# Kernel optimization log

Hardware: AMD Instinct MI355X
Metric: run time of the kernel (lower is better)

The kernel has to match this reference:

```python
import jax, jax.numpy as jnp
import numpy as np

EPS = 1e-5

def setup_inputs() -> dict:
    key = jax.random.key(0)
    ks = jax.random.split(key, 8)
    B, T, D, S = 8, 4096, 1024, 64
    return {
        "x": jax.random.normal(ks[0], (B, T, D), dtype=jnp.float32),
        "time_decay": jax.random.normal(ks[1], (S,), dtype=jnp.float32) * 0.1 - 0.5,
        "time_first": jax.random.normal(ks[2], (S,), dtype=jnp.float32) * 0.1,
        "W_key": jax.random.normal(ks[3], (S, D), dtype=jnp.float32) * 0.02,
        "W_value": jax.random.normal(ks[4], (S, D), dtype=jnp.float32) * 0.02,
        "W_output": jax.random.normal(ks[5], (D, S), dtype=jnp.float32) * 0.02,
        "W_shift": jax.random.normal(ks[6], (D, D), dtype=jnp.float32) * 0.02,
        "shift_gate": jnp.ones((D,), dtype=jnp.float32),
        "ln_w": jnp.ones((D,), dtype=jnp.float32),
        "ln_b": jnp.zeros((D,), dtype=jnp.float32),
    }


def _forward(x, time_decay, time_first, W_key, W_value, W_output, W_shift, shift_gate, ln_w, ln_b):
    B, T, D = x.shape
    S = time_decay.shape[0]
    # --- token shift: rotate sequence by shift_len, project, gated blend ---
    shift_len = max(1, int(T * 0.5))
    x_cat = jnp.concatenate([x[:, shift_len:], x[:, :-shift_len]], axis=1)  # (B,T,D)
    gate = jax.nn.sigmoid(shift_gate)
    x_shift = jnp.einsum('btd,ed->bte', x_cat, W_shift) * gate + x * (1.0 - gate)
    # --- layernorm (torch: biased variance, eps=1e-5) ---
    mu = jnp.mean(x_shift, axis=-1, keepdims=True)
    var = jnp.mean(jnp.square(x_shift - mu), axis=-1, keepdims=True)
    xn = (x_shift - mu) * jax.lax.rsqrt(var + EPS) * ln_w + ln_b
    # --- key/value projections and per-step wkv (fully vectorized) ---
    k = jnp.einsum('btd,sd->bts', xn, W_key)    # (B,T,S)
    v = jnp.einsum('btd,sd->bts', xn, W_value)  # (B,T,S)
    wkv = jnp.exp(-jnp.exp(time_first) * jax.nn.sigmoid(k)) * v  # (B,T,S)
    # --- linear recurrence: state = state*w + wkv_t, scanned over T ---
    w = jnp.exp(time_decay)  # (S,)
    def step(state, wkv_t):
        state = state * w + wkv_t
        return state, state
    init = jnp.zeros((B, S), dtype=x.dtype)
    last_state, states = jax.lax.scan(step, init, jnp.swapaxes(wkv, 0, 1))  # states: (T,B,S)
    states = jnp.swapaxes(states, 0, 1)  # (B,T,S)
    # --- batched output projection (applied per-step in torch; same math) ---
    output = jnp.einsum('bts,ds->btd', states, W_output)  # (B,T,D)
    return output, last_state


def reference(x, time_decay, time_first, W_key, W_value, W_output, W_shift, shift_gate, ln_w, ln_b):
    out, last_state = _forward(x, time_decay, time_first, W_key, W_value, W_output, W_shift, shift_gate, ln_w, ln_b)
    return out, jax.lax.stop_gradient(last_state)
```

## Files before the change

kernel.cpp:

```cpp
#include <hip/hip_runtime.h>
#include <stdint.h>

#define B_ 8
#define T_ 4096
#define D_ 1024
#define S_ 64
#define N_ 32768
#define OUT_ELEMS 33554432
#define NCHK 128
#define CHKL 32

typedef __attribute__((ext_vector_type(8))) short bf16x8;
typedef __attribute__((ext_vector_type(8))) unsigned short u16x8;
typedef __attribute__((ext_vector_type(4))) float f32x4;

__device__ __forceinline__ uint16_t f2bf(float f) {
    union { float f; uint32_t u; } v; v.f = f;
    uint32_t r = v.u + 0x7FFFu + ((v.u >> 16) & 1u);
    return (uint16_t)(r >> 16);
}
__device__ __forceinline__ float bf2f(uint16_t h) {
    union { uint32_t u; float f; } v; v.u = ((uint32_t)h) << 16;
    return v.f;
}

#define GLOAD_LDS16(gp, lp)                                             \
    __builtin_amdgcn_global_load_lds(                                   \
        (const __attribute__((address_space(1))) void*)(gp),            \
        (__attribute__((address_space(3))) void*)(lp), 16, 0, 0)

__global__ void prep(const float* __restrict__ x,
                     const float* __restrict__ Wsf, const float* __restrict__ Wkf,
                     const float* __restrict__ Wvf, const float* __restrict__ Wof,
                     const float* __restrict__ sg, const float* __restrict__ tf,
                     const float* __restrict__ lnw, const float* __restrict__ lnb,
                     uint16_t* __restrict__ xb, uint16_t* __restrict__ Wsb,
                     uint16_t* __restrict__ Wkvb, uint16_t* __restrict__ Wob,
                     float* __restrict__ gbuf, float* __restrict__ efirst,
                     float* __restrict__ ucvec, float* __restrict__ rowstats)
{
    __shared__ float red[4];
    const int blk = blockIdx.x, tid = threadIdx.x;
    if (blk < 2048) {
        for (int i = blk * 256 + tid; i < OUT_ELEMS / 4; i += 2048 * 256) {
            float4 v = ((const float4*)x)[i];
            ushort4 o;
            o.x = f2bf(v.x); o.y = f2bf(v.y); o.z = f2bf(v.z); o.w = f2bf(v.w);
            ((ushort4*)xb)[i] = o;
        }
        return;
    }
    if (blk < 3298) {
        int i = (blk - 2048) * 256 + tid;
        const float* src; uint16_t* dst; int j; bool fold = false;
        if (i < 262144) { src = Wsf; dst = Wsb; j = i; }
        else if (i < 278528) { src = Wkf; dst = Wkvb; j = i - 262144; fold = true; }
        else if (i < 294912) { src = Wvf; dst = Wkvb + 65536; j = i - 278528; fold = true; }
        else if (i < 311296) { src = Wof; dst = Wob; j = i - 294912; }
        else if (i < 311552) {
            j = i - 311296;
            float4 v = ((const float4*)sg)[j];
            float4 g;
            g.x = 1.f / (1.f + __expf(-v.x)); g.y = 1.f / (1.f + __expf(-v.y));
            g.z = 1.f / (1.f + __expf(-v.z)); g.w = 1.f / (1.f + __expf(-v.w));
            ((float4*)gbuf)[j] = g;
            return;
        } else if (i < 311568) {
            j = i - 311552;
            float4 v = ((const float4*)tf)[j];
            float4 e;
            e.x = __expf(v.x); e.y = __expf(v.y); e.z = __expf(v.z); e.w = __expf(v.w);
            ((float4*)efirst)[j] = e;
            return;
        } else return;
        float4 v = ((const float4*)src)[j];
        if (fold) {
            float4 l = ((const float4*)lnw)[j & 255];
            v.x *= l.x; v.y *= l.y; v.z *= l.z; v.w *= l.w;
        }
        ushort4 o;
        o.x = f2bf(v.x); o.y = f2bf(v.y); o.z = f2bf(v.z); o.w = f2bf(v.w);
        ((ushort4*)dst)[j] = o;
        return;
    }
    if (blk < 3554) {
        int b2 = blk - 3298;
        int which = b2 >> 6, s = b2 & 63;
        const float* W = (which < 2) ? Wkf : Wvf;
        const float* L = (which & 1) ? lnb : lnw;
        float4 wv = ((const float4*)W)[s * 256 + tid];
        float4 lv = ((const float4*)L)[tid];
        float p = wv.x * lv.x + wv.y * lv.y + wv.z * lv.z + wv.w * lv.w;
#pragma unroll
        for (int off = 32; off; off >>= 1) p += __shfl_xor(p, off);
        if ((tid & 63) == 0) red[tid >> 6] = p;
        __syncthreads();
        if (tid == 0) ucvec[which * 64 + s] = red[0] + red[1] + red[2] + red[3];
        return;
    }
    {
        int i = (blk - 3554) * 256 + tid;
        float4 z; z.x = 0.f; z.y = 0.f; z.z = 0.f; z.w = 0.f;
        ((float4*)rowstats)[i] = z;
    }
}

__global__ __launch_bounds__(256) void k1_shift_gemm(
    const uint16_t* __restrict__ xb, const uint16_t* __restrict__ Wsb,
    const float* __restrict__ gbuf, uint16_t* __restrict__ xs,
    float* __restrict__ rowstats)
{
    __shared__ char sh[34816];
    uint16_t (*As)[64] = (uint16_t(*)[64])sh;
    uint16_t (*Bs)[64] = (uint16_t(*)[64])(sh + 16384);
    float (*epi)[68] = (float(*)[68])sh;

    const int tid = threadIdx.x;
    const int w = tid >> 6, lane = tid & 63, quad = lane >> 4, l16 = lane & 15;
    const int wm = w >> 1, wn = w & 1;
    const int lin = blockIdx.x;
    const int mt = (lin & 7) * 32 + (lin >> 6);
    const int nt = (lin >> 3) & 7;
    const int m0 = mt * 128, n0 = nt * 128;
    const int m0x = m0 ^ 2048;

    const int srow = w * 32 + (lane >> 3);
    const int scg  = ((lane & 7) ^ ((lane >> 3) & 7)) * 8;
    const uint16_t* aG = xb  + (size_t)(m0x + srow) * D_ + scg;
    const uint16_t* bG = Wsb + (size_t)(n0  + srow) * D_ + scg;

    f32x4 acc[4][4];
#pragma unroll
    for (int i = 0; i < 4; ++i)
#pragma unroll
        for (int j = 0; j < 4; ++j) acc[i][j] = (f32x4){0.f, 0.f, 0.f, 0.f};

    for (int k0 = 0; k0 < D_; k0 += 64) {
        __syncthreads();
#pragma unroll
        for (int i = 0; i < 4; ++i) {
            GLOAD_LDS16(aG + k0 + (size_t)(i * 8) * D_, &As[w * 32 + i * 8][0]);
            GLOAD_LDS16(bG + k0 + (size_t)(i * 8) * D_, &Bs[w * 32 + i * 8][0]);
        }
        __syncthreads();
#pragma unroll
        for (int ks = 0; ks < 2; ++ks) {
            bf16x8 a[4], b[4];
#pragma unroll
            for (int i = 0; i < 4; ++i)
                a[i] = *(const bf16x8*)&As[wm * 64 + i * 16 + l16]
                                         [(((ks * 4 + quad) ^ (l16 & 7)) * 8)];
#pragma unroll
            for (int j = 0; j < 4; ++j)
                b[j] = *(const bf16x8*)&Bs[wn * 64 + j * 16 + l16]
                                         [(((ks * 4 + quad) ^ (l16 & 7)) * 8)];
#pragma unroll
            for (int i = 0; i < 4; ++i)
#pragma unroll
                for (int j = 0; j < 4; ++j)
                    acc[i][j] = __builtin_amdgcn_mfma_f32_16x16x32_bf16(
                        a[i], b[j], acc[i][j], 0, 0, 0);
        }
    }

    const int row = tid >> 1;
    const int c0 = (tid & 1) * 32;
#pragma unroll
    for (int h = 0; h < 2; ++h) {
        __syncthreads();
        if (wn == h) {
#pragma unroll
            for (int i = 0; i < 4; ++i)
#pragma unroll
                for (int j = 0; j < 4; ++j)
#pragma unroll
                    for (int r = 0; r < 4; ++r)
                        epi[wm * 64 + i * 16 + quad * 4 + r][j * 16 + l16] =
                            acc[i][j][r];
        }
        __syncthreads();
        const int col = n0 + h * 64 + c0;
        const uint16_t* xrow = xb + (size_t)(m0 + row) * D_ + col;
        uint16_t* orow = xs + (size_t)(m0 + row) * D_ + col;
        float sr = 0.f, qr = 0.f;
#pragma unroll
        for (int c4 = 0; c4 < 8; ++c4) {
            float4 g4 = ((const float4*)(gbuf + col))[c4];
            ushort4 xh = ((const ushort4*)xrow)[c4];
            const float* e = &epi[row][c0 + c4 * 4];
            float b0 = e[0] * g4.x + bf2f(xh.x) * (1.f - g4.x);
            float b1 = e[1] * g4.y + bf2f(xh.y) * (1.f - g4.y);
            float b2 = e[2] * g4.z + bf2f(xh.z) * (1.f - g4.z);
            float b3 = e[3] * g4.w + bf2f(xh.w) * (1.f - g4.w);
            ushort4 o;
            o.x = f2bf(b0); o.y = f2bf(b1); o.z = f2bf(b2); o.w = f2bf(b3);
            ((ushort4*)orow)[c4] = o;
            sr += (b0 + b1) + (b2 + b3);
            qr += (b0 * b0 + b1 * b1) + (b2 * b2 + b3 * b3);
        }
        sr += __shfl_xor(sr, 1);
        qr += __shfl_xor(qr, 1);
        if ((lane & 1) == 0) {
            float* rs = rowstats + (size_t)(m0 + row) * 2;
            atomicAdd(rs, sr);
            atomicAdd(rs + 1, qr);
        }
    }
}

__global__ __launch_bounds__(256) void k3_kv(
    const uint16_t* __restrict__ xsb, const uint16_t* __restrict__ Wkvb,
    const float* __restrict__ efirst, const float* __restrict__ rowstats,
    const float* __restrict__ ucvec, float* __restrict__ wkv)
{
    __shared__ char sh[33792];
    uint16_t (*As)[64] = (uint16_t(*)[64])sh;
    uint16_t (*Bs)[64] = (uint16_t(*)[64])(sh + 8192);
    float (*epi)[132] = (float(*)[132])sh;

    const int tid = threadIdx.x;
    const int w = tid >> 6, lane = tid & 63, quad = lane >> 4, l16 = lane & 15;
    const int wm = w >> 1, wn = w & 1;
    const int m0 = blockIdx.x * 64;

    const int lrow = w * 8 + (lane >> 3);
    const int scg  = ((lane & 7) ^ ((lane >> 3) & 7)) * 8;
    const uint16_t* aG = xsb + (size_t)(m0 + lrow) * D_ + scg;
    const uint16_t* bG = Wkvb + (size_t)lrow * D_ + scg;

    f32x4 acc[2][4];
#pragma unroll
    for (int i = 0; i < 2; ++i)
#pragma unroll
        for (int j = 0; j < 4; ++j) acc[i][j] = (f32x4){0.f, 0.f, 0.f, 0.f};

    for (int k0 = 0; k0 < D_; k0 += 64) {
        __syncthreads();
#pragma unroll
        for (int i = 0; i < 2; ++i)
            GLOAD_LDS16(aG + k0 + (size_t)(i * 32) * D_, &As[w * 8 + i * 32][0]);
#pragma unroll
        for (int i = 0; i < 4; ++i)
            GLOAD_LDS16(bG + k0 + (size_t)(i * 32) * D_, &Bs[w * 8 + i * 32][0]);
        __syncthreads();
#pragma unroll
        for (int ks = 0; ks < 2; ++ks) {
            bf16x8 a[2], b[4];
#pragma unroll
            for (int i = 0; i < 2; ++i)
                a[i] = *(const bf16x8*)&As[wm * 32 + i * 16 + l16]
                                         [(((ks * 4 + quad) ^ (l16 & 7)) * 8)];
#pragma unroll
            for (int j = 0; j < 4; ++j)
                b[j] = *(const bf16x8*)&Bs[wn * 64 + j * 16 + l16]
                                         [(((ks * 4 + quad) ^ (l16 & 7)) * 8)];
#pragma unroll
            for (int i = 0; i < 2; ++i)
#pragma unroll
                for (int j = 0; j < 4; ++j)
                    acc[i][j] = __builtin_amdgcn_mfma_f32_16x16x32_bf16(
                        a[i], b[j], acc[i][j], 0, 0, 0);
        }
    }

    __syncthreads();
#pragma unroll
    for (int i = 0; i < 2; ++i)
#pragma unroll
        for (int j = 0; j < 4; ++j)
#pragma unroll
            for (int r = 0; r < 4; ++r)
                epi[wm * 32 + i * 16 + quad * 4 + r][wn * 64 + j * 16 + l16] =
                    acc[i][j][r];
    __syncthreads();

    const int row = tid >> 2, s0 = (tid & 3) * 16;
    const float2 rs = ((const float2*)rowstats)[m0 + row];
    const float mu = rs.x * (1.f / (float)D_);
    const float var = rs.y * (1.f / (float)D_) - mu * mu;
    const float rstd = rsqrtf(var + 1e-5f);
    float* dst = wkv + (size_t)(m0 + row) * S_ + s0;
#pragma unroll
    for (int c4 = 0; c4 < 4; ++c4) {
        float4 kk = *(const float4*)&epi[row][s0 + c4 * 4];
        float4 vv = *(const float4*)&epi[row][64 + s0 + c4 * 4];
        float4 uk4 = *(const float4*)(ucvec + 0 * 64 + s0 + c4 * 4);
        float4 ck4 = *(const float4*)(ucvec + 1 * 64 + s0 + c4 * 4);
        float4 uv4 = *(const float4*)(ucvec + 2 * 64 + s0 + c4 * 4);
        float4 cv4 = *(const float4*)(ucvec + 3 * 64 + s0 + c4 * 4);
        float4 ef = ((const float4*)(efirst + s0))[c4];
        float kx = rstd * (kk.x - mu * uk4.x) + ck4.x;
        float ky = rstd * (kk.y - mu * uk4.y) + ck4.y;
        float kz = rstd * (kk.z - mu * uk4.z) + ck4.z;
        float kw = rstd * (kk.w - mu * uk4.w) + ck4.w;
        float vx = rstd * (vv.x - mu * uv4.x) + cv4.x;
        float vy = rstd * (vv.y - mu * uv4.y) + cv4.y;
        float vz = rstd * (vv.z - mu * uv4.z) + cv4.z;
        float vw = rstd * (vv.w - mu * uv4.w) + cv4.w;
        float4 o;
        o.x = __expf(-ef.x / (1.f + __expf(-kx))) * vx;
        o.y = __expf(-ef.y / (1.f + __expf(-ky))) * vy;
        o.z = __expf(-ef.z / (1.f + __expf(-kz))) * vz;
        o.w = __expf(-ef.w / (1.f + __expf(-kw))) * vw;
        *(float4*)(dst + c4 * 4) = o;
    }
}

__global__ void k4a(const float* __restrict__ wkv,
                    const float* __restrict__ time_decay,
                    float* __restrict__ part)
{
    const int s = threadIdx.x;
    const int bc = blockIdx.x;
    const int b = bc >> 7, c = bc & (NCHK - 1);
    float w = expf(time_decay[s]);
    const float* src = wkv + ((size_t)b * T_ + c * CHKL) * S_ + s;
    float st = 0.f;
#pragma unroll
    for (int t = 0; t < CHKL; ++t) st = st * w + src[(size_t)t * S_];
    part[(size_t)bc * S_ + s] = st;
}
__global__ void k4bc(const float* __restrict__ wkv,
                     const float* __restrict__ time_decay,
                     const float* __restrict__ part,
                     uint16_t* __restrict__ stb,
                     float* __restrict__ last_state)
{
    const int s = threadIdx.x;
    const int bc = blockIdx.x;
    const int b = bc >> 7, c = bc & (NCHK - 1);
    const float td = time_decay[s];
    const float w = expf(td);
    const float wL = expf(td * (float)CHKL);
    const float* pp = part + (size_t)b * NCHK * S_ + s;
    float cin = 0.f;
#pragma unroll 4
    for (int j = 0; j < c; ++j) cin = cin * wL + pp[(size_t)j * S_];
    const float* src = wkv + ((size_t)b * T_ + c * CHKL) * S_ + s;
    uint16_t* dst = stb + ((size_t)b * T_ + c * CHKL) * S_ + s;
    float st = cin;
#pragma unroll
    for (int t = 0; t < CHKL; ++t) {
        st = st * w + src[(size_t)t * S_];
        dst[(size_t)t * S_] = f2bf(st);
    }
    if (c == NCHK - 1) last_state[b * S_ + s] = st;
}

__global__ __launch_bounds__(256) void k5_out(
    const uint16_t* __restrict__ st, const uint16_t* __restrict__ Wob,
    float* __restrict__ out)
{
    __shared__ float epi[128][68];
    const int tid = threadIdx.x;
    const int w = tid >> 6, lane = tid & 63, quad = lane >> 4, l16 = lane & 15;
    const int wm = w >> 1, wn = w & 1;
    const int m0b = blockIdx.y * 128;
    const int n0b = blockIdx.x * 128;

    f32x4 acc[4][4];
#pragma unroll
    for (int i = 0; i < 4; ++i)
#pragma unroll
        for (int j = 0; j < 4; ++j) acc[i][j] = (f32x4){0.f, 0.f, 0.f, 0.f};

#pragma unroll
    for (int k = 0; k < S_; k += 32) {
        bf16x8 a[4], b[4];
#pragma unroll
        for (int i = 0; i < 4; ++i)
            a[i] = *(const bf16x8*)(st + (size_t)(m0b + wm * 64 + i * 16 + l16) * S_ + k + quad * 8);
#pragma unroll
        for (int i = 0; i < 4; ++i)
            b[i] = *(const bf16x8*)(Wob + (size_t)(n0b + wn * 64 + i * 16 + l16) * S_ + k + quad * 8);
#pragma unroll
        for (int i = 0; i < 4; ++i)
#pragma unroll
            for (int j = 0; j < 4; ++j)
                acc[i][j] = __builtin_amdgcn_mfma_f32_16x16x32_bf16(
                    a[i], b[j], acc[i][j], 0, 0, 0);
    }

    const int row = tid >> 1;
    const int c0 = (tid & 1) * 32;
#pragma unroll
    for (int h = 0; h < 2; ++h) {
        __syncthreads();
        if (wn == h) {
#pragma unroll
            for (int i = 0; i < 4; ++i)
#pragma unroll
                for (int j = 0; j < 4; ++j)
#pragma unroll
                    for (int r = 0; r < 4; ++r)
                        epi[wm * 64 + i * 16 + quad * 4 + r][j * 16 + l16] =
                            acc[i][j][r];
        }
        __syncthreads();
        float* dst = out + (size_t)(m0b + row) * D_ + n0b + h * 64 + c0;
#pragma unroll
        for (int c4 = 0; c4 < 8; ++c4)
            ((float4*)dst)[c4] = *(const float4*)&epi[row][c0 + c4 * 4];
    }
}

extern "C" void kernel_launch(void* const* d_in, const int* in_sizes, int n_in,
                              void* d_out, int out_size, void* d_ws, size_t ws_size,
                              hipStream_t stream) {
    const float* x          = (const float*)d_in[0];
    const float* time_decay = (const float*)d_in[1];
    const float* time_first = (const float*)d_in[2];
    const float* W_key      = (const float*)d_in[3];
    const float* W_value    = (const float*)d_in[4];
    const float* W_output   = (const float*)d_in[5];
    const float* W_shift    = (const float*)d_in[6];
    const float* shift_gate = (const float*)d_in[7];
    const float* ln_w       = (const float*)d_in[8];
    const float* ln_b       = (const float*)d_in[9];
    float* out = (float*)d_out;

    char* ws = (char*)d_ws;
    uint16_t* xb      = (uint16_t*)(ws + 0);
    uint16_t* xs      = (uint16_t*)(ws + 67108864);
    float*    wkv     = (float*)   (ws + 134217728);
    uint16_t* stb     = (uint16_t*)(ws + 142606336);
    uint16_t* Wsb     = (uint16_t*)(ws + 146800640);
    uint16_t* Wkvb    = (uint16_t*)(ws + 148897792);
    uint16_t* Wob     = (uint16_t*)(ws + 149159936);
    float*    part    = (float*)   (ws + 149291008);
    float*    rowstats= (float*)   (ws + 149553152);
    float*    gbuf    = (float*)   (ws + 149815296);
    float*    efirst  = (float*)   (ws + 149819392);
    float*    ucvec   = (float*)   (ws + 149819648);

    prep<<<3618, 256, 0, stream>>>(x, W_shift, W_key, W_value, W_output,
                                   shift_gate, time_first, ln_w, ln_b,
                                   xb, Wsb, Wkvb, Wob, gbuf, efirst,
                                   ucvec, rowstats);
    k1_shift_gemm<<<2048, 256, 0, stream>>>(xb, Wsb, gbuf, xs, rowstats);
    k3_kv<<<512, 256, 0, stream>>>(xs, Wkvb, efirst, rowstats, ucvec, wkv);
    k4a<<<B_ * NCHK, S_, 0, stream>>>(wkv, time_decay, part);
    k4bc<<<B_ * NCHK, S_, 0, stream>>>(wkv, time_decay, part, stb, out + OUT_ELEMS);
    k5_out<<<dim3(8, 256), 256, 0, stream>>>(stb, Wob, out);
}
```

Before: 429.0 us.

## Compute layernorm row stats in KV kernel via MFMA instead of atomics

Removes the per-row sum and sum-of-squares accumulation and global atomics from the shift GEMM epilogue, along with the prep blocks that zeroed the stats buffer. The KV GEMM now derives the row statistics itself with extra MFMAs on the A tiles it already loads: one against a vector of ones for the sum, and one of each tile against itself, whose diagonal gives the sum of squares. The results go to shared memory. This cuts atomic traffic and epilogue work in the larger kernel at the cost of a few extra MFMAs. The statistics are now taken from the bf16-rounded shifted activations rather than fp32 values.

```diff
diff --git a/kernel.cpp b/kernel.cpp
--- a/kernel.cpp
+++ b/kernel.cpp
@@ -37,7 +37,7 @@
                      uint16_t* __restrict__ xb, uint16_t* __restrict__ Wsb,
                      uint16_t* __restrict__ Wkvb, uint16_t* __restrict__ Wob,
                      float* __restrict__ gbuf, float* __restrict__ efirst,
-                     float* __restrict__ ucvec, float* __restrict__ rowstats)
+                     float* __restrict__ ucvec)
 {
     __shared__ float red[4];
     const int blk = blockIdx.x, tid = threadIdx.x;
@@ -83,7 +83,7 @@
         ((ushort4*)dst)[j] = o;
         return;
     }
-    if (blk < 3554) {
+    {
         int b2 = blk - 3298;
         int which = b2 >> 6, s = b2 & 63;
         const float* W = (which < 2) ? Wkf : Wvf;
@@ -96,19 +96,12 @@
         if ((tid & 63) == 0) red[tid >> 6] = p;
         __syncthreads();
         if (tid == 0) ucvec[which * 64 + s] = red[0] + red[1] + red[2] + red[3];
-        return;
-    }
-    {
-        int i = (blk - 3554) * 256 + tid;
-        float4 z; z.x = 0.f; z.y = 0.f; z.z = 0.f; z.w = 0.f;
-        ((float4*)rowstats)[i] = z;
     }
 }
 
 __global__ __launch_bounds__(256) void k1_shift_gemm(
     const uint16_t* __restrict__ xb, const uint16_t* __restrict__ Wsb,
-    const float* __restrict__ gbuf, uint16_t* __restrict__ xs,
-    float* __restrict__ rowstats)
+    const float* __restrict__ gbuf, uint16_t* __restrict__ xs)
 {
     __shared__ char sh[34816];
     uint16_t (*As)[64] = (uint16_t(*)[64])sh;
@@ -182,41 +175,32 @@
         const int col = n0 + h * 64 + c0;
         const uint16_t* xrow = xb + (size_t)(m0 + row) * D_ + col;
         uint16_t* orow = xs + (size_t)(m0 + row) * D_ + col;
-        float sr = 0.f, qr = 0.f;
 #pragma unroll
         for (int c4 = 0; c4 < 8; ++c4) {
             float4 g4 = ((const float4*)(gbuf + col))[c4];
             ushort4 xh = ((const ushort4*)xrow)[c4];
             const float* e = &epi[row][c0 + c4 * 4];
-            float b0 = e[0] * g4.x + bf2f(xh.x) * (1.f - g4.x);
-            float b1 = e[1] * g4.y + bf2f(xh.y) * (1.f - g4.y);
-            float b2 = e[2] * g4.z + bf2f(xh.z) * (1.f - g4.z);
-            float b3 = e[3] * g4.w + bf2f(xh.w) * (1.f - g4.w);
             ushort4 o;
-            o.x = f2bf(b0); o.y = f2bf(b1); o.z = f2bf(b2); o.w = f2bf(b3);
+            o.x = f2bf(e[0] * g4.x + bf2f(xh.x) * (1.f - g4.x));
+            o.y = f2bf(e[1] * g4.y + bf2f(xh.y) * (1.f - g4.y));
+            o.z = f2bf(e[2] * g4.z + bf2f(xh.z) * (1.f - g4.z));
+            o.w = f2bf(e[3] * g4.w + bf2f(xh.w) * (1.f - g4.w));
             ((ushort4*)orow)[c4] = o;
-            sr += (b0 + b1) + (b2 + b3);
-            qr += (b0 * b0 + b1 * b1) + (b2 * b2 + b3 * b3);
-        }
-        sr += __shfl_xor(sr, 1);
-        qr += __shfl_xor(qr, 1);
-        if ((lane & 1) == 0) {
-            float* rs = rowstats + (size_t)(m0 + row) * 2;
-            atomicAdd(rs, sr);
-            atomicAdd(rs + 1, qr);
         }
     }
 }
 
 __global__ __launch_bounds__(256) void k3_kv(
     const uint16_t* __restrict__ xsb, const uint16_t* __restrict__ Wkvb,
-    const float* __restrict__ efirst, const float* __restrict__ rowstats,
-    const float* __restrict__ ucvec, float* __restrict__ wkv)
-{
-    __shared__ char sh[33792];
+    const float* __restrict__ efirst, const float* __restrict__ ucvec,
+    float* __restrict__ wkv)
+{
+    __shared__ char sh[34816];
     uint16_t (*As)[64] = (uint16_t(*)[64])sh;
     uint16_t (*Bs)[64] = (uint16_t(*)[64])(sh + 8192);
     float (*epi)[132] = (float(*)[132])sh;
+    float* ssh = (float*)(sh + 33792);
+    float* qsh = (float*)(sh + 34048);
 
     const int tid = threadIdx.x;
     const int w = tid >> 6, lane = tid & 63, quad = lane >> 4, l16 = lane & 15;
@@ -233,6 +217,15 @@
     for (int i = 0; i < 2; ++i)
 #pragma unroll
         for (int j = 0; j < 4; ++j) acc[i][j] = (f32x4){0.f, 0.f, 0.f, 0.f};
+    f32x4 accs[2], accq[2];
+#pragma unroll
+    for (int i = 0; i < 2; ++i) {
+        accs[i] = (f32x4){0.f, 0.f, 0.f, 0.f};
+        accq[i] = (f32x4){0.f, 0.f, 0.f, 0.f};
+    }
+    bf16x8 ones;
+#pragma unroll
+    for (int j = 0; j < 8; ++j) ones[j] = (short)0x3F80;
 
     for (int k0 = 0; k0 < D_; k0 += 64) {
         __syncthreads();
@@ -260,6 +253,28 @@
                 for (int j = 0; j < 4; ++j)
                     acc[i][j] = __builtin_amdgcn_mfma_f32_16x16x32_bf16(
                         a[i], b[j], acc[i][j], 0, 0, 0);
+            if (wn == 0) {
+#pragma unroll
+                for (int i = 0; i < 2; ++i) {
+                    accs[i] = __builtin_amdgcn_mfma_f32_16x16x32_bf16(
+                        a[i], ones, accs[i], 0, 0, 0);
+                    accq[i] = __builtin_amdgcn_mfma_f32_16x16x32_bf16(
+                        a[i], a[i], accq[i], 0, 0, 0);
+                }
+            }
+        }
+    }
+
+    if (wn == 0) {
+#pragma unroll
+        for (int i = 0; i < 2; ++i) {
+            if (l16 == 0) {
+#pragma unroll
+                for (int r = 0; r < 4; ++r)
+                    ssh[wm * 32 + i * 16 + quad * 4 + r] = accs[i][r];
+            }
+            if ((l16 >> 2) == quad)
+                qsh[wm * 32 + i * 16 + l16] = accq[i][l16 & 3];
         }
     }
 
@@ -275,9 +290,8 @@
     __syncthreads();
 
     const int row = tid >> 2, s0 = (tid & 3) * 16;
-    const float2 rs = ((const float2*)rowstats)[m0 + row];
-    const float mu = rs.x * (1.f / (float)D_);
-    const float var = rs.y * (1.f / (float)D_) - mu * mu;
+    const float mu = ssh[row] * (1.f / (float)D_);
+    const float var = qsh[row] * (1.f / (float)D_) - mu * mu;
     const float rstd = rsqrtf(var + 1e-5f);
     float* dst = wkv + (size_t)(m0 + row) * S_ + s0;
 #pragma unroll
@@ -428,17 +442,15 @@
     uint16_t* Wkvb    = (uint16_t*)(ws + 148897792);
     uint16_t* Wob     = (uint16_t*)(ws + 149159936);
     float*    part    = (float*)   (ws + 149291008);
-    float*    rowstats= (float*)   (ws + 149553152);
     float*    gbuf    = (float*)   (ws + 149815296);
     float*    efirst  = (float*)   (ws + 149819392);
     float*    ucvec   = (float*)   (ws + 149819648);
 
-    prep<<<3618, 256, 0, stream>>>(x, W_shift, W_key, W_value, W_output,
+    prep<<<3554, 256, 0, stream>>>(x, W_shift, W_key, W_value, W_output,
                                    shift_gate, time_first, ln_w, ln_b,
-                                   xb, Wsb, Wkvb, Wob, gbuf, efirst,
-                                   ucvec, rowstats);
-    k1_shift_gemm<<<2048, 256, 0, stream>>>(xb, Wsb, gbuf, xs, rowstats);
-    k3_kv<<<512, 256, 0, stream>>>(xs, Wkvb, efirst, rowstats, ucvec, wkv);
+                                   xb, Wsb, Wkvb, Wob, gbuf, efirst, ucvec);
+    k1_shift_gemm<<<2048, 256, 0, stream>>>(xb, Wsb, gbuf, xs);
+    k3_kv<<<512, 256, 0, stream>>>(xs, Wkvb, efirst, ucvec, wkv);
     k4a<<<B_ * NCHK, S_, 0, stream>>>(wkv, time_decay, part);
     k4bc<<<B_ * NCHK, S_, 0, stream>>>(wkv, time_decay, part, stb, out + OUT_ELEMS);
     k5_out<<<dim3(8, 256), 256, 0, stream>>>(stb, Wob, out);
```

New measurement: 436.4 us. About the same (+1.7%).
